# Performance work log

Measured on AMD Instinct MI355X. Metric: run time of the kernel, lower is better.

Reference implementation:

```python
import jax, jax.numpy as jnp
import numpy as np

B, N, C, H = 2, 4096, 256, 4
DH = C // H  # 64
EPS = 1e-6
TEMPERATURE = 1.0


def setup_inputs() -> dict:
    key = jax.random.key(0)
    ks = jax.random.split(key, 12)
    s = 0.02
    return {
        "x": jax.random.normal(ks[0], (B, N, C), dtype=jnp.float32),
        "pos_embed": jax.random.normal(ks[1], (B, N, C), dtype=jnp.float32),
        # per-head Q/K/V linear weights stacked over heads (torch Linear(dim, dim_head))
        "Wq": jax.random.normal(ks[2], (H, C, DH), dtype=jnp.float32) * s,
        "bq": jax.random.normal(ks[3], (H, DH), dtype=jnp.float32) * s,
        "Wk": jax.random.normal(ks[4], (H, C, DH), dtype=jnp.float32) * s,
        "bk": jax.random.normal(ks[5], (H, DH), dtype=jnp.float32) * s,
        "Wv": jax.random.normal(ks[6], (H, C, DH), dtype=jnp.float32) * s,
        "bv": jax.random.normal(ks[7], (H, DH), dtype=jnp.float32) * s,
        "Wo": jax.random.normal(ks[8], (C, C), dtype=jnp.float32) * s,
        "bo": jax.random.normal(ks[9], (C,), dtype=jnp.float32) * s,
        "ln_g": jnp.ones((C,), dtype=jnp.float32),
        "ln_b": jnp.zeros((C,), dtype=jnp.float32),
    }


def reference(x, pos_embed, Wq, bq, Wk, bk, Wv, bv, Wo, bo, ln_g, ln_b):
    dk = TEMPERATURE * jnp.sqrt(jnp.float32(DH))
    # pre-norm: x + pos_embed -> dropout(p=0, identity) -> LayerNorm(eps=1e-6)
    h = x + pos_embed
    mu = jnp.mean(h, axis=-1, keepdims=True)
    var = jnp.mean(jnp.square(h - mu), axis=-1, keepdims=True)
    h = (h - mu) * jax.lax.rsqrt(var + EPS) * ln_g + ln_b  # [B,N,C]
    # all heads at once (original loops over heads with separate small Linears)
    q = jnp.einsum("bnc,hcd->bhnd", h, Wq) + bq[None, :, None, :]
    k = jnp.einsum("bnc,hcd->bhnd", h, Wk) + bk[None, :, None, :]
    v = jnp.einsum("bnc,hcd->bhnd", h, Wv) + bv[None, :, None, :]
    scores = jnp.einsum("bhid,bhjd->bhij", q, k) / dk  # [B,H,N,N]
    # NOTE: original uses F.softmax(dot_prod, dim=1) on [B,N,N] -> normalize over
    # the QUERY axis i, not the key axis j. Replicated faithfully here (axis=2).
    attn = jax.nn.softmax(scores, axis=2)
    o = jnp.einsum("bhij,bhjd->bhid", attn, v)  # [B,H,N,DH]
    o = jnp.transpose(o, (0, 2, 1, 3)).reshape(B, N, C)  # concat heads on channel
    return o @ Wo + bo
```

## Files before the change

### kernel.cpp

```cpp
#include <hip/hip_runtime.h>
#include <math.h>

#define B_ 2
#define N_ 4096
#define C_ 256
#define H_ 4
#define DH_ 64
#define EPS_ 1e-6f
#define SCALE_Q_ 0.18033688011112042f

typedef short bf16x8 __attribute__((ext_vector_type(8)));
typedef float f32x4 __attribute__((ext_vector_type(4)));
typedef int i32x4 __attribute__((ext_vector_type(4)));

#define MFMA32(a, b, c) __builtin_amdgcn_mfma_f32_16x16x32_bf16(a, b, c, 0, 0, 0)
#define FAST_EXP2(x) __builtin_amdgcn_exp2f(x)

__device__ __forceinline__ unsigned short f2bf(float x) {
  unsigned int u = __float_as_uint(x);
  return (unsigned short)((u + 0x7FFFu + ((u >> 16) & 1u)) >> 16);
}
__device__ __forceinline__ float bf2f(unsigned short u) {
  return __uint_as_float(((unsigned int)u) << 16);
}
__device__ __forceinline__ int pack2bf(float lo, float hi) {
  return (int)__builtin_amdgcn_perm(__float_as_uint(hi) + 0x8000u,
                                    __float_as_uint(lo) + 0x8000u, 0x07060302u);
}

__global__ __launch_bounds__(256) void ln_kernel(
    const float* __restrict__ x, const float* __restrict__ pos,
    const float* __restrict__ g, const float* __restrict__ beta,
    unsigned short* __restrict__ h16) {
  const int row = blockIdx.x;
  const int t = threadIdx.x;
  const int w = t >> 6;
  float val = x[row * C_ + t] + pos[row * C_ + t];
  __shared__ float sm[8];
  float s = val;
  s += __shfl_xor(s, 1);  s += __shfl_xor(s, 2);  s += __shfl_xor(s, 4);
  s += __shfl_xor(s, 8);  s += __shfl_xor(s, 16); s += __shfl_xor(s, 32);
  if ((t & 63) == 0) sm[w] = s;
  __syncthreads();
  const float mu = (sm[0] + sm[1] + sm[2] + sm[3]) * (1.0f / C_);
  const float d = val - mu;
  float v = d * d;
  v += __shfl_xor(v, 1);  v += __shfl_xor(v, 2);  v += __shfl_xor(v, 4);
  v += __shfl_xor(v, 8);  v += __shfl_xor(v, 16); v += __shfl_xor(v, 32);
  if ((t & 63) == 0) sm[4 + w] = v;
  __syncthreads();
  const float var = (sm[4] + sm[5] + sm[6] + sm[7]) * (1.0f / C_);
  h16[row * C_ + t] = f2bf(d * rsqrtf(var + EPS_) * g[t] + beta[t]);
}

__global__ __launch_bounds__(256) void wconv_kernel(
    const float* __restrict__ Wq, const float* __restrict__ Wk,
    const float* __restrict__ Wv, const float* __restrict__ Wo,
    unsigned short* __restrict__ W3T, unsigned short* __restrict__ WoT) {
  const int base = blockIdx.x * 2048;
#pragma unroll
  for (int p = 0; p < 8; p++) {
    const int idx = base + p * 256 + threadIdx.x;
    if (idx < 196608) {
      const int m = idx >> 14;
      const int rem = idx & 16383;
      const int c = rem >> 6, d = rem & 63;
      const int h = m / 3, kind = m - h * 3;
      const float* W = kind == 0 ? Wq : kind == 1 ? Wk : Wv;
      float v = W[h * 16384 + rem];
      if (kind == 0) v *= SCALE_Q_;
      W3T[(h * 192 + kind * 64 + d) * 256 + c] = f2bf(v);
    } else {
      const int widx = idx - 196608;
      const int k = widx >> 8, n = widx & 255;
      WoT[n * 256 + k] = f2bf(Wo[widx]);
    }
  }
}

__global__ __launch_bounds__(256) void qkv_kernel(
    const unsigned short* __restrict__ h16, const unsigned short* __restrict__ W3T,
    const float* __restrict__ bq, const float* __restrict__ bk,
    const float* __restrict__ bv,
    unsigned short* __restrict__ q16, unsigned short* __restrict__ k16,
    unsigned short* __restrict__ vT16) {
  const int rt = blockIdx.x;
  const int hh = blockIdx.y;
  const int t = threadIdx.x;
  const int w = t >> 6, lane = t & 63, c = lane & 15, quad = lane >> 4;
  __shared__ unsigned short Hs[128 * 64];
  __shared__ unsigned short Bs[192 * 64];
  const int row0 = rt * 128;

  f32x4 acc[2][12];
#pragma unroll
  for (int mi = 0; mi < 2; mi++)
#pragma unroll
    for (int nt = 0; nt < 12; nt++) acc[mi][nt] = (f32x4){0.f, 0.f, 0.f, 0.f};

  for (int kt = 0; kt < C_; kt += 64) {
    __syncthreads();
#pragma unroll
    for (int p = 0; p < 4; p++) {
      const int e = t + p * 256;
      const int row = e >> 3, ch = e & 7;
      *(bf16x8*)&Hs[row * 64 + ((ch ^ (row & 7)) * 8)] =
          *(const bf16x8*)&h16[(size_t)(row0 + row) * C_ + kt + ch * 8];
    }
#pragma unroll
    for (int p = 0; p < 6; p++) {
      const int e = t + p * 256;
      const int row = e >> 3, ch = e & 7;
      *(bf16x8*)&Bs[row * 64 + ((ch ^ (row & 7)) * 8)] =
          *(const bf16x8*)&W3T[(size_t)(hh * 192 + row) * C_ + kt + ch * 8];
    }
    __syncthreads();
#pragma unroll
    for (int kh = 0; kh < 2; kh++) {
      bf16x8 a[2];
#pragma unroll
      for (int mi = 0; mi < 2; mi++) {
        const int i = w * 32 + mi * 16 + c;
        a[mi] = *(const bf16x8*)&Hs[i * 64 + (((kh * 4 + quad) ^ (i & 7)) * 8)];
      }
#pragma unroll
      for (int nt = 0; nt < 12; nt++) {
        const int n = nt * 16 + c;
        bf16x8 b = *(const bf16x8*)&Bs[n * 64 + (((kh * 4 + quad) ^ (n & 7)) * 8)];
        acc[0][nt] = MFMA32(a[0], b, acc[0][nt]);
        acc[1][nt] = MFMA32(a[1], b, acc[1][nt]);
      }
    }
  }
#pragma unroll
  for (int nt = 0; nt < 12; nt++) {
    const int kind = nt >> 2;
    const int col = (nt & 3) * 16 + c;
    const float bias = kind == 0 ? bq[hh * 64 + col] * SCALE_Q_
                     : kind == 1 ? bk[hh * 64 + col] : bv[hh * 64 + col];
#pragma unroll
    for (int mi = 0; mi < 2; mi++) {
#pragma unroll
      for (int r = 0; r < 4; r++) {
        const int gr = row0 + w * 32 + mi * 16 + quad * 4 + r;
        const int b = gr >> 12, n = gr & (N_ - 1);
        const size_t bh = (size_t)(b * H_ + hh);
        const unsigned short val = f2bf(acc[mi][nt][r] + bias);
        if (kind == 0)      q16[(bh * N_ + n) * DH_ + col] = val;
        else if (kind == 1) k16[(bh * N_ + n) * DH_ + col] = val;
        else                vT16[(bh * DH_ + col) * N_ + n] = val;
      }
    }
  }
}

__global__ __launch_bounds__(256, 2) void colstats_kernel(
    const unsigned short* __restrict__ q16, const unsigned short* __restrict__ k16,
    unsigned short* __restrict__ vT16) {
  const int blk = blockIdx.x;
  const int bh = blk & 7;
  const int j0 = (blk >> 3) * 64;
  const int t = threadIdx.x;
  const int w = t >> 6, lane = t & 63, c = lane & 15, quad = lane >> 4;
  __shared__ unsigned short Qs[64 * 64];
  __shared__ float Lp[4][64];
  __shared__ float ilv[64];

  bf16x8 ka[4][2];
#pragma unroll
  for (int jb = 0; jb < 4; jb++) {
    const size_t kb = ((size_t)bh * N_ + j0 + jb * 16 + c) * DH_;
    ka[jb][0] = *(const bf16x8*)&k16[kb + quad * 8];
    ka[jb][1] = *(const bf16x8*)&k16[kb + 32 + quad * 8];
  }

  bf16x8 pre[2];
  auto loadQ = [&](int i0) {
#pragma unroll
    for (int p = 0; p < 2; p++) {
      const int e = t + p * 256;
      const int row = e >> 3, ch = e & 7;
      pre[p] = *(const bf16x8*)&q16[((size_t)bh * N_ + i0 + row) * DH_ + ch * 8];
    }
  };
  loadQ(0);

  f32x4 lsum[4];
#pragma unroll
  for (int jb = 0; jb < 4; jb++) lsum[jb] = (f32x4){0.f, 0.f, 0.f, 0.f};

  for (int i0 = 0; i0 < N_; i0 += 64) {
    __syncthreads();
#pragma unroll
    for (int p = 0; p < 2; p++) {
      const int e = t + p * 256;
      const int row = e >> 3, ch = e & 7;
      *(bf16x8*)&Qs[row * 64 + ((ch ^ (row & 7)) * 8)] = pre[p];
    }
    __syncthreads();
    if (i0 + 64 < N_) loadQ(i0 + 64);
    const int ir = w * 16 + c;
    bf16x8 qf0 = *(const bf16x8*)&Qs[ir * 64 + ((quad ^ (c & 7)) * 8)];
    bf16x8 qf1 = *(const bf16x8*)&Qs[ir * 64 + (((4 + quad) ^ (c & 7)) * 8)];
#pragma unroll
    for (int jb = 0; jb < 4; jb++) {
      f32x4 s = {0.f, 0.f, 0.f, 0.f};
      s = MFMA32(ka[jb][0], qf0, s);
      s = MFMA32(ka[jb][1], qf1, s);
#pragma unroll
      for (int r = 0; r < 4; r++) lsum[jb][r] += FAST_EXP2(s[r]);
    }
  }
#pragma unroll
  for (int jb = 0; jb < 4; jb++) {
#pragma unroll
    for (int r = 0; r < 4; r++) {
      float s = lsum[jb][r];
      s += __shfl_xor(s, 1); s += __shfl_xor(s, 2);
      s += __shfl_xor(s, 4); s += __shfl_xor(s, 8);
      if (c == 0) Lp[w][jb * 16 + quad * 4 + r] = s;
    }
  }
  __syncthreads();
  if (t < 64) ilv[t] = 1.0f / (Lp[0][t] + Lp[1][t] + Lp[2][t] + Lp[3][t]);
  __syncthreads();
#pragma unroll
  for (int p = 0; p < 2; p++) {
    const int e = t + p * 256;
    const int d = e >> 3, ch = e & 7;
    const size_t addr = ((size_t)bh * DH_ + d) * N_ + j0 + ch * 8;
    bf16x8 v = *(const bf16x8*)&vT16[addr];
#pragma unroll
    for (int jj = 0; jj < 8; jj++)
      v[jj] = (short)f2bf(bf2f((unsigned short)v[jj]) * ilv[ch * 8 + jj]);
    *(bf16x8*)&vT16[addr] = v;
  }
}

__global__ __launch_bounds__(512, 4) void attnout_kernel(
    const unsigned short* __restrict__ q16, const unsigned short* __restrict__ k16,
    const unsigned short* __restrict__ vT16, unsigned short* __restrict__ ob16) {
  const int blk = blockIdx.x;
  const int bh = blk & 7;
  const int bb = bh >> 2, hh = bh & 3;
  const int i0 = (blk >> 3) * 64;
  const int t = threadIdx.x;
  const int w = t >> 6, lane = t & 63, c = lane & 15, quad = lane >> 4;
  const int iw = w >> 2;
  const int jw = w & 3;

  __shared__ __align__(16) char smem[32768];
  unsigned short* Ks = (unsigned short*)smem;
  unsigned short* Vs = (unsigned short*)smem + 128 * 64;
  float* Rf = (float*)smem;

  bf16x8 qa[2][2];
#pragma unroll
  for (int ib = 0; ib < 2; ib++) {
    const size_t qb = ((size_t)bh * N_ + i0 + iw * 32 + ib * 16 + c) * DH_;
    qa[ib][0] = *(const bf16x8*)&q16[qb + quad * 8];
    qa[ib][1] = *(const bf16x8*)&q16[qb + 32 + quad * 8];
  }

  bf16x8 kpre[2], vpre[2];
  auto loadKV = [&](int jt) {
#pragma unroll
    for (int p = 0; p < 2; p++) {
      const int e = t + p * 512;
      kpre[p] = *(const bf16x8*)&k16[((size_t)bh * N_ + jt + (e >> 3)) * DH_ + (e & 7) * 8];
      vpre[p] = *(const bf16x8*)&vT16[((size_t)bh * DH_ + (e >> 4)) * N_ + jt + (e & 15) * 8];
    }
  };
  loadKV(0);

  f32x4 of[2][4];
#pragma unroll
  for (int ib = 0; ib < 2; ib++)
#pragma unroll
    for (int dt = 0; dt < 4; dt++) of[ib][dt] = (f32x4){0.f, 0.f, 0.f, 0.f};

  for (int jt = 0; jt < N_; jt += 128) {
    __syncthreads();
#pragma unroll
    for (int p = 0; p < 2; p++) {
      const int e = t + p * 512;
      { const int row = e >> 3, ch = e & 7;
        *(bf16x8*)&Ks[row * 64 + ((ch ^ ((row >> 2) & 7)) * 8)] = kpre[p]; }
      { const int d = e >> 4, ch = e & 15;
        *(bf16x8*)&Vs[d * 128 + ((ch ^ (d & 15)) * 8)] = vpre[p]; }
    }
    __syncthreads();
    if (jt + 128 < N_) loadKV(jt + 128);

    bf16x8 kf[2][2];
#pragma unroll
    for (int s = 0; s < 2; s++) {
      const int jr = jw * 32 + ((c >> 2) * 8) + s * 4 + (c & 3);
      const int swz = (jr >> 2) & 7;
      kf[s][0] = *(const bf16x8*)&Ks[jr * 64 + ((quad ^ swz) * 8)];
      kf[s][1] = *(const bf16x8*)&Ks[jr * 64 + (((4 + quad) ^ swz) * 8)];
    }
    bf16x8 vf[4];
#pragma unroll
    for (int dt = 0; dt < 4; dt++) {
      const int d = dt * 16 + c;
      vf[dt] = *(const bf16x8*)&Vs[d * 128 + (((jw * 4 + quad) ^ (d & 15)) * 8)];
    }

#pragma unroll
    for (int ib = 0; ib < 2; ib++) {
      f32x4 s0 = {0.f, 0.f, 0.f, 0.f}, s1 = {0.f, 0.f, 0.f, 0.f};
      s0 = MFMA32(kf[0][0], qa[ib][0], s0);
      s0 = MFMA32(kf[0][1], qa[ib][1], s0);
      s1 = MFMA32(kf[1][0], qa[ib][0], s1);
      s1 = MFMA32(kf[1][1], qa[ib][1], s1);
      i32x4 pi;
      pi[0] = pack2bf(FAST_EXP2(s0[0]), FAST_EXP2(s0[1]));
      pi[1] = pack2bf(FAST_EXP2(s0[2]), FAST_EXP2(s0[3]));
      pi[2] = pack2bf(FAST_EXP2(s1[0]), FAST_EXP2(s1[1]));
      pi[3] = pack2bf(FAST_EXP2(s1[2]), FAST_EXP2(s1[3]));
      bf16x8 pf = *(bf16x8*)&pi;
#pragma unroll
      for (int dt = 0; dt < 4; dt++)
        of[ib][dt] = MFMA32(pf, vf[dt], of[ib][dt]);
    }
  }

  __syncthreads();
  if (jw >= 2) {
    float* dst = Rf + (iw * 2 + (jw - 2)) * 2048;
#pragma unroll
    for (int ib = 0; ib < 2; ib++)
#pragma unroll
      for (int dt = 0; dt < 4; dt++)
        *(f32x4*)&dst[lane * 32 + (((ib * 4 + dt) ^ (lane & 7)) * 4)] = of[ib][dt];
  }
  __syncthreads();
  if (jw < 2) {
    const float* src = Rf + (iw * 2 + jw) * 2048;
#pragma unroll
    for (int ib = 0; ib < 2; ib++)
#pragma unroll
      for (int dt = 0; dt < 4; dt++)
        of[ib][dt] += *(const f32x4*)&src[lane * 32 + (((ib * 4 + dt) ^ (lane & 7)) * 4)];
  }
  __syncthreads();
  if (jw == 1) {
    float* dst = Rf + iw * 2048;
#pragma unroll
    for (int ib = 0; ib < 2; ib++)
#pragma unroll
      for (int dt = 0; dt < 4; dt++)
        *(f32x4*)&dst[lane * 32 + (((ib * 4 + dt) ^ (lane & 7)) * 4)] = of[ib][dt];
  }
  __syncthreads();
  if (jw == 0) {
    const float* src = Rf + iw * 2048;
#pragma unroll
    for (int ib = 0; ib < 2; ib++)
#pragma unroll
      for (int dt = 0; dt < 4; dt++) {
        of[ib][dt] += *(const f32x4*)&src[lane * 32 + (((ib * 4 + dt) ^ (lane & 7)) * 4)];
#pragma unroll
        for (int r = 0; r < 4; r++)
          ob16[((size_t)bb * N_ + i0 + iw * 32 + ib * 16 + quad * 4 + r) * C_ +
               hh * DH_ + dt * 16 + c] = f2bf(of[ib][dt][r]);
      }
  }
}

__global__ __launch_bounds__(256) void outproj_kernel(
    const unsigned short* __restrict__ ob16, const unsigned short* __restrict__ WoT,
    const float* __restrict__ bo, float* __restrict__ out) {
  const int rt = blockIdx.x;
  const int t = threadIdx.x;
  const int w = t >> 6, lane = t & 63, c = lane & 15, quad = lane >> 4;
  __shared__ unsigned short As[32 * 64];
  __shared__ unsigned short Bs[256 * 64];

  f32x4 acc[2][4];
#pragma unroll
  for (int mt = 0; mt < 2; mt++)
#pragma unroll
    for (int nt = 0; nt < 4; nt++) acc[mt][nt] = (f32x4){0.f, 0.f, 0.f, 0.f};

  for (int kt = 0; kt < C_; kt += 64) {
    __syncthreads();
    {
      const int row = t >> 3, ch = t & 7;
      *(bf16x8*)&As[row * 64 + ((ch ^ (row & 7)) * 8)] =
          *(const bf16x8*)&ob16[((size_t)rt * 32 + row) * C_ + kt + ch * 8];
    }
#pragma unroll
    for (int p = 0; p < 8; p++) {
      const int e = t + p * 256;
      const int row = e >> 3, ch = e & 7;
      *(bf16x8*)&Bs[row * 64 + ((ch ^ (row & 7)) * 8)] =
          *(const bf16x8*)&WoT[(size_t)row * C_ + kt + ch * 8];
    }
    __syncthreads();
#pragma unroll
    for (int kh = 0; kh < 2; kh++) {
      bf16x8 a[2];
#pragma unroll
      for (int mt = 0; mt < 2; mt++) {
        const int i = mt * 16 + c;
        a[mt] = *(const bf16x8*)&As[i * 64 + (((kh * 4 + quad) ^ (i & 7)) * 8)];
      }
#pragma unroll
      for (int nt = 0; nt < 4; nt++) {
        const int n = w * 64 + nt * 16 + c;
        bf16x8 b = *(const bf16x8*)&Bs[n * 64 + (((kh * 4 + quad) ^ (n & 7)) * 8)];
        acc[0][nt] = MFMA32(a[0], b, acc[0][nt]);
        acc[1][nt] = MFMA32(a[1], b, acc[1][nt]);
      }
    }
  }
#pragma unroll
  for (int mt = 0; mt < 2; mt++)
#pragma unroll
    for (int nt = 0; nt < 4; nt++) {
      const int col = w * 64 + nt * 16 + c;
      const float bias = bo[col];
#pragma unroll
      for (int r = 0; r < 4; r++)
        out[((size_t)rt * 32 + mt * 16 + quad * 4 + r) * C_ + col] = acc[mt][nt][r] + bias;
    }
}

extern "C" void kernel_launch(void* const* d_in, const int* in_sizes, int n_in,
                              void* d_out, int out_size, void* d_ws, size_t ws_size,
                              hipStream_t stream) {
  const float* x    = (const float*)d_in[0];
  const float* pos  = (const float*)d_in[1];
  const float* Wq   = (const float*)d_in[2];
  const float* bq   = (const float*)d_in[3];
  const float* Wk   = (const float*)d_in[4];
  const float* bk   = (const float*)d_in[5];
  const float* Wv   = (const float*)d_in[6];
  const float* bv   = (const float*)d_in[7];
  const float* Wo   = (const float*)d_in[8];
  const float* bo   = (const float*)d_in[9];
  const float* ln_g = (const float*)d_in[10];
  const float* ln_b = (const float*)d_in[11];
  float* out = (float*)d_out;

  const size_t SZ = (size_t)B_ * N_ * C_;
  unsigned short* h16  = (unsigned short*)d_ws;
  unsigned short* q16  = h16 + SZ;
  unsigned short* k16  = q16 + SZ;
  unsigned short* vT16 = k16 + SZ;
  unsigned short* ob16 = vT16 + SZ;
  unsigned short* W3T  = ob16 + SZ;
  unsigned short* WoT  = W3T + (size_t)H_ * 192 * 256;

  ln_kernel<<<B_ * N_, 256, 0, stream>>>(x, pos, ln_g, ln_b, h16);
  wconv_kernel<<<128, 256, 0, stream>>>(Wq, Wk, Wv, Wo, W3T, WoT);
  qkv_kernel<<<dim3(64, H_), 256, 0, stream>>>(h16, W3T, bq, bk, bv, q16, k16, vT16);
  colstats_kernel<<<512, 256, 0, stream>>>(q16, k16, vT16);
  attnout_kernel<<<512, 512, 0, stream>>>(q16, k16, vT16, ob16);
  outproj_kernel<<<256, 256, 0, stream>>>(ob16, WoT, bo, out);
}
```

Baseline: 190.5 us.

## Rework LN, QKV and colstats kernels for more blocks and less syncing

LayerNorm now handles one row per wavefront with float4 loads, so it needs no shared memory or block barriers, and launches a quarter as many blocks. The QKV GEMM tile shrinks from 128 to 64 rows, doubling the grid. Colstats now covers 32 keys per block, again doubling the grid, and reads Q fragments straight from global memory instead of staging them through LDS with barriers. The goal is better occupancy and fewer syncs, at the cost of more redundant global Q reads in colstats and less reuse of the weight tile in QKV.

```diff
diff --git a/kernel.cpp b/kernel.cpp
--- a/kernel.cpp
+++ b/kernel.cpp
@@ -10,6 +10,7 @@
 #define SCALE_Q_ 0.18033688011112042f
 
 typedef short bf16x8 __attribute__((ext_vector_type(8)));
+typedef short bf16x4v __attribute__((ext_vector_type(4)));
 typedef float f32x4 __attribute__((ext_vector_type(4)));
 typedef int i32x4 __attribute__((ext_vector_type(4)));
 
@@ -32,25 +33,28 @@
     const float* __restrict__ x, const float* __restrict__ pos,
     const float* __restrict__ g, const float* __restrict__ beta,
     unsigned short* __restrict__ h16) {
-  const int row = blockIdx.x;
-  const int t = threadIdx.x;
-  const int w = t >> 6;
-  float val = x[row * C_ + t] + pos[row * C_ + t];
-  __shared__ float sm[8];
-  float s = val;
+  const int w = threadIdx.x >> 6, lane = threadIdx.x & 63;
+  const int row = blockIdx.x * 4 + w;
+  const float4 xv = *(const float4*)&x[row * C_ + lane * 4];
+  const float4 pv = *(const float4*)&pos[row * C_ + lane * 4];
+  float4 v = {xv.x + pv.x, xv.y + pv.y, xv.z + pv.z, xv.w + pv.w};
+  float s = v.x + v.y + v.z + v.w;
   s += __shfl_xor(s, 1);  s += __shfl_xor(s, 2);  s += __shfl_xor(s, 4);
   s += __shfl_xor(s, 8);  s += __shfl_xor(s, 16); s += __shfl_xor(s, 32);
-  if ((t & 63) == 0) sm[w] = s;
-  __syncthreads();
-  const float mu = (sm[0] + sm[1] + sm[2] + sm[3]) * (1.0f / C_);
-  const float d = val - mu;
-  float v = d * d;
-  v += __shfl_xor(v, 1);  v += __shfl_xor(v, 2);  v += __shfl_xor(v, 4);
-  v += __shfl_xor(v, 8);  v += __shfl_xor(v, 16); v += __shfl_xor(v, 32);
-  if ((t & 63) == 0) sm[4 + w] = v;
-  __syncthreads();
-  const float var = (sm[4] + sm[5] + sm[6] + sm[7]) * (1.0f / C_);
-  h16[row * C_ + t] = f2bf(d * rsqrtf(var + EPS_) * g[t] + beta[t]);
+  const float mu = s * (1.0f / C_);
+  float4 d = {v.x - mu, v.y - mu, v.z - mu, v.w - mu};
+  float q = d.x * d.x + d.y * d.y + d.z * d.z + d.w * d.w;
+  q += __shfl_xor(q, 1);  q += __shfl_xor(q, 2);  q += __shfl_xor(q, 4);
+  q += __shfl_xor(q, 8);  q += __shfl_xor(q, 16); q += __shfl_xor(q, 32);
+  const float rs = rsqrtf(q * (1.0f / C_) + EPS_);
+  const float4 g4 = *(const float4*)&g[lane * 4];
+  const float4 b4 = *(const float4*)&beta[lane * 4];
+  bf16x4v o;
+  o[0] = (short)f2bf(d.x * rs * g4.x + b4.x);
+  o[1] = (short)f2bf(d.y * rs * g4.y + b4.y);
+  o[2] = (short)f2bf(d.z * rs * g4.z + b4.z);
+  o[3] = (short)f2bf(d.w * rs * g4.w + b4.w);
+  *(bf16x4v*)&h16[row * C_ + lane * 4] = o;
 }
 
 __global__ __launch_bounds__(256) void wconv_kernel(
@@ -88,20 +92,18 @@
   const int hh = blockIdx.y;
   const int t = threadIdx.x;
   const int w = t >> 6, lane = t & 63, c = lane & 15, quad = lane >> 4;
-  __shared__ unsigned short Hs[128 * 64];
+  __shared__ unsigned short Hs[64 * 64];
   __shared__ unsigned short Bs[192 * 64];
-  const int row0 = rt * 128;
-
-  f32x4 acc[2][12];
-#pragma unroll
-  for (int mi = 0; mi < 2; mi++)
-#pragma unroll
-    for (int nt = 0; nt < 12; nt++) acc[mi][nt] = (f32x4){0.f, 0.f, 0.f, 0.f};
+  const int row0 = rt * 64;
+
+  f32x4 acc[12];
+#pragma unroll
+  for (int nt = 0; nt < 12; nt++) acc[nt] = (f32x4){0.f, 0.f, 0.f, 0.f};
 
   for (int kt = 0; kt < C_; kt += 64) {
     __syncthreads();
 #pragma unroll
-    for (int p = 0; p < 4; p++) {
+    for (int p = 0; p < 2; p++) {
       const int e = t + p * 256;
       const int row = e >> 3, ch = e & 7;
       *(bf16x8*)&Hs[row * 64 + ((ch ^ (row & 7)) * 8)] =
@@ -117,18 +119,13 @@
     __syncthreads();
 #pragma unroll
     for (int kh = 0; kh < 2; kh++) {
-      bf16x8 a[2];
-#pragma unroll
-      for (int mi = 0; mi < 2; mi++) {
-        const int i = w * 32 + mi * 16 + c;
-        a[mi] = *(const bf16x8*)&Hs[i * 64 + (((kh * 4 + quad) ^ (i & 7)) * 8)];
-      }
+      const int i = w * 16 + c;
+      bf16x8 a = *(const bf16x8*)&Hs[i * 64 + (((kh * 4 + quad) ^ (i & 7)) * 8)];
 #pragma unroll
       for (int nt = 0; nt < 12; nt++) {
         const int n = nt * 16 + c;
         bf16x8 b = *(const bf16x8*)&Bs[n * 64 + (((kh * 4 + quad) ^ (n & 7)) * 8)];
-        acc[0][nt] = MFMA32(a[0], b, acc[0][nt]);
-        acc[1][nt] = MFMA32(a[1], b, acc[1][nt]);
+        acc[nt] = MFMA32(a, b, acc[nt]);
       }
     }
   }
@@ -139,80 +136,59 @@
     const float bias = kind == 0 ? bq[hh * 64 + col] * SCALE_Q_
                      : kind == 1 ? bk[hh * 64 + col] : bv[hh * 64 + col];
 #pragma unroll
-    for (int mi = 0; mi < 2; mi++) {
-#pragma unroll
-      for (int r = 0; r < 4; r++) {
-        const int gr = row0 + w * 32 + mi * 16 + quad * 4 + r;
-        const int b = gr >> 12, n = gr & (N_ - 1);
-        const size_t bh = (size_t)(b * H_ + hh);
-        const unsigned short val = f2bf(acc[mi][nt][r] + bias);
-        if (kind == 0)      q16[(bh * N_ + n) * DH_ + col] = val;
-        else if (kind == 1) k16[(bh * N_ + n) * DH_ + col] = val;
-        else                vT16[(bh * DH_ + col) * N_ + n] = val;
-      }
-    }
-  }
-}
-
-__global__ __launch_bounds__(256, 2) void colstats_kernel(
+    for (int r = 0; r < 4; r++) {
+      const int gr = row0 + w * 16 + quad * 4 + r;
+      const int b = gr >> 12, n = gr & (N_ - 1);
+      const size_t bh = (size_t)(b * H_ + hh);
+      const unsigned short val = f2bf(acc[nt][r] + bias);
+      if (kind == 0)      q16[(bh * N_ + n) * DH_ + col] = val;
+      else if (kind == 1) k16[(bh * N_ + n) * DH_ + col] = val;
+      else                vT16[(bh * DH_ + col) * N_ + n] = val;
+    }
+  }
+}
+
+__global__ __launch_bounds__(256, 4) void colstats_kernel(
     const unsigned short* __restrict__ q16, const unsigned short* __restrict__ k16,
     unsigned short* __restrict__ vT16) {
   const int blk = blockIdx.x;
   const int bh = blk & 7;
-  const int j0 = (blk >> 3) * 64;
+  const int j0 = (blk >> 3) * 32;
   const int t = threadIdx.x;
   const int w = t >> 6, lane = t & 63, c = lane & 15, quad = lane >> 4;
-  __shared__ unsigned short Qs[64 * 64];
-  __shared__ float Lp[4][64];
-  __shared__ float ilv[64];
-
-  bf16x8 ka[4][2];
-#pragma unroll
-  for (int jb = 0; jb < 4; jb++) {
+  __shared__ float Lp[4][32];
+  __shared__ float ilv[32];
+
+  bf16x8 ka[2][2];
+#pragma unroll
+  for (int jb = 0; jb < 2; jb++) {
     const size_t kb = ((size_t)bh * N_ + j0 + jb * 16 + c) * DH_;
     ka[jb][0] = *(const bf16x8*)&k16[kb + quad * 8];
     ka[jb][1] = *(const bf16x8*)&k16[kb + 32 + quad * 8];
   }
 
-  bf16x8 pre[2];
-  auto loadQ = [&](int i0) {
-#pragma unroll
-    for (int p = 0; p < 2; p++) {
-      const int e = t + p * 256;
-      const int row = e >> 3, ch = e & 7;
-      pre[p] = *(const bf16x8*)&q16[((size_t)bh * N_ + i0 + row) * DH_ + ch * 8];
-    }
-  };
-  loadQ(0);
-
-  f32x4 lsum[4];
-#pragma unroll
-  for (int jb = 0; jb < 4; jb++) lsum[jb] = (f32x4){0.f, 0.f, 0.f, 0.f};
-
-  for (int i0 = 0; i0 < N_; i0 += 64) {
-    __syncthreads();
-#pragma unroll
-    for (int p = 0; p < 2; p++) {
-      const int e = t + p * 256;
-      const int row = e >> 3, ch = e & 7;
-      *(bf16x8*)&Qs[row * 64 + ((ch ^ (row & 7)) * 8)] = pre[p];
-    }
-    __syncthreads();
-    if (i0 + 64 < N_) loadQ(i0 + 64);
-    const int ir = w * 16 + c;
-    bf16x8 qf0 = *(const bf16x8*)&Qs[ir * 64 + ((quad ^ (c & 7)) * 8)];
-    bf16x8 qf1 = *(const bf16x8*)&Qs[ir * 64 + (((4 + quad) ^ (c & 7)) * 8)];
-#pragma unroll
-    for (int jb = 0; jb < 4; jb++) {
-      f32x4 s = {0.f, 0.f, 0.f, 0.f};
-      s = MFMA32(ka[jb][0], qf0, s);
-      s = MFMA32(ka[jb][1], qf1, s);
-#pragma unroll
-      for (int r = 0; r < 4; r++) lsum[jb][r] += FAST_EXP2(s[r]);
-    }
-  }
-#pragma unroll
-  for (int jb = 0; jb < 4; jb++) {
+  f32x4 lsum[2];
+#pragma unroll
+  for (int jb = 0; jb < 2; jb++) lsum[jb] = (f32x4){0.f, 0.f, 0.f, 0.f};
+
+  for (int i0 = 0; i0 < N_; i0 += 256) {
+#pragma unroll
+    for (int is = 0; is < 4; is++) {
+      const size_t qb = ((size_t)bh * N_ + i0 + w * 64 + is * 16 + c) * DH_;
+      bf16x8 qf0 = *(const bf16x8*)&q16[qb + quad * 8];
+      bf16x8 qf1 = *(const bf16x8*)&q16[qb + 32 + quad * 8];
+#pragma unroll
+      for (int jb = 0; jb < 2; jb++) {
+        f32x4 s = {0.f, 0.f, 0.f, 0.f};
+        s = MFMA32(ka[jb][0], qf0, s);
+        s = MFMA32(ka[jb][1], qf1, s);
+#pragma unroll
+        for (int r = 0; r < 4; r++) lsum[jb][r] += FAST_EXP2(s[r]);
+      }
+    }
+  }
+#pragma unroll
+  for (int jb = 0; jb < 2; jb++) {
 #pragma unroll
     for (int r = 0; r < 4; r++) {
       float s = lsum[jb][r];
@@ -222,12 +198,10 @@
     }
   }
   __syncthreads();
-  if (t < 64) ilv[t] = 1.0f / (Lp[0][t] + Lp[1][t] + Lp[2][t] + Lp[3][t]);
-  __syncthreads();
-#pragma unroll
-  for (int p = 0; p < 2; p++) {
-    const int e = t + p * 256;
-    const int d = e >> 3, ch = e & 7;
+  if (t < 32) ilv[t] = 1.0f / (Lp[0][t] + Lp[1][t] + Lp[2][t] + Lp[3][t]);
+  __syncthreads();
+  {
+    const int d = t >> 2, ch = t & 3;
     const size_t addr = ((size_t)bh * DH_ + d) * N_ + j0 + ch * 8;
     bf16x8 v = *(const bf16x8*)&vT16[addr];
 #pragma unroll
@@ -454,10 +428,10 @@
   unsigned short* W3T  = ob16 + SZ;
   unsigned short* WoT  = W3T + (size_t)H_ * 192 * 256;
 
-  ln_kernel<<<B_ * N_, 256, 0, stream>>>(x, pos, ln_g, ln_b, h16);
+  ln_kernel<<<B_ * N_ / 4, 256, 0, stream>>>(x, pos, ln_g, ln_b, h16);
   wconv_kernel<<<128, 256, 0, stream>>>(Wq, Wk, Wv, Wo, W3T, WoT);
-  qkv_kernel<<<dim3(64, H_), 256, 0, stream>>>(h16, W3T, bq, bk, bv, q16, k16, vT16);
-  colstats_kernel<<<512, 256, 0, stream>>>(q16, k16, vT16);
+  qkv_kernel<<<dim3(128, H_), 256, 0, stream>>>(h16, W3T, bq, bk, bv, q16, k16, vT16);
+  colstats_kernel<<<1024, 256, 0, stream>>>(q16, k16, vT16);
   attnout_kernel<<<512, 512, 0, stream>>>(q16, k16, vT16, ob16);
   outproj_kernel<<<256, 256, 0, stream>>>(ob16, WoT, bo, out);
 }
```

New measurement: 213.0 us. 1.12x slower.
